# Optimization experiments

Measured on AMD Instinct MI355X. Metric: run time of the kernel, lower is better.

Reference implementation:

```python
import jax, jax.numpy as jnp
import numpy as np

N_EMBED = 1024
N_HEADS = 16
HEAD_DIM = N_EMBED // N_HEADS


def setup_inputs() -> dict:
    key = jax.random.key(0)
    ks = jax.random.split(key, 5)
    B, T, C = 4, 2048, N_EMBED
    s_in = 1.0 / np.sqrt(C)
    x = jax.random.normal(ks[0], (B, T, C), dtype=jnp.float32)
    W_qkv = jax.random.normal(ks[1], (C, 3 * C), dtype=jnp.float32) * s_in
    b_qkv = jnp.zeros((3 * C,), dtype=jnp.float32)
    W_out = jax.random.normal(ks[2], (C, C), dtype=jnp.float32) * s_in
    b_out = jnp.zeros((C,), dtype=jnp.float32)
    return {"x": x, "W_qkv": W_qkv, "b_qkv": b_qkv, "W_out": W_out, "b_out": b_out}


def reference(x, W_qkv, b_qkv, W_out, b_out):
    B, T, C = x.shape
    H, D = N_HEADS, HEAD_DIM
    qkv = x @ W_qkv + b_qkv                       # [B,T,3C]
    q, k, v = jnp.split(qkv, 3, axis=-1)
    # [B,T,C] -> [B,H,T,D]
    q = q.reshape(B, T, H, D).transpose(0, 2, 1, 3)
    k = k.reshape(B, T, H, D).transpose(0, 2, 1, 3)
    v = v.reshape(B, T, H, D).transpose(0, 2, 1, 3)
    scale = 1.0 / np.sqrt(D)
    attn = jnp.einsum('bhqd,bhkd->bhqk', q, k) * scale   # [B,H,T,T]
    causal = jnp.tril(jnp.ones((T, T), dtype=bool))
    attn = jnp.where(causal, attn, -jnp.inf)
    attn = jax.nn.softmax(attn, axis=-1)
    out = jnp.einsum('bhqk,bhkd->bhqd', attn, v)          # [B,H,T,D]
    out = out.transpose(0, 2, 1, 3).reshape(B, T, C)
    return out @ W_out + b_out
```

## Files before the change

kernel.cpp:

```cpp
#include <hip/hip_runtime.h>
#include <stdint.h>

#define BB 4
#define TT 2048
#define CC 1024
#define HH 16
#define DD 64
#define MM (BB*TT)

typedef __bf16 bf16x8 __attribute__((ext_vector_type(8)));
typedef float  f32x4  __attribute__((ext_vector_type(4)));

__device__ __forceinline__ unsigned short f2bf(float f) {
  __bf16 h = (__bf16)f;
  union { __bf16 h; unsigned short u; } c; c.h = h;
  return c.u;
}

__device__ __forceinline__ void glds16(const void* g, void* l) {
  __builtin_amdgcn_global_load_lds((const __attribute__((address_space(1))) void*)g,
                                   (__attribute__((address_space(3))) void*)l,
                                   16, 0, 0);
}

__device__ __forceinline__ int xcd_swz(int bid, int nwg) {
  if (nwg & 7) return bid;
  return (bid & 7) * (nwg >> 3) + (bid >> 3);
}

typedef unsigned short u16x8 __attribute__((ext_vector_type(8)));
__global__ void f32_to_bf16_kn(const float* __restrict__ in,
                               unsigned short* __restrict__ out, int n) {
  int i = (blockIdx.x * blockDim.x + threadIdx.x) * 8;
  const int stride = gridDim.x * blockDim.x * 8;
  for (; i < n; i += stride) {
    float4 a = *(const float4*)&in[i];
    float4 b = *(const float4*)&in[i + 4];
    u16x8 t;
    t[0]=f2bf(a.x); t[1]=f2bf(a.y); t[2]=f2bf(a.z); t[3]=f2bf(a.w);
    t[4]=f2bf(b.x); t[5]=f2bf(b.y); t[6]=f2bf(b.z); t[7]=f2bf(b.w);
    *(u16x8*)&out[i] = t;
  }
}

__global__ void transpose_to_bf16(const float* __restrict__ in,
                                  unsigned short* __restrict__ out,
                                  int R, int Cc) {
  __shared__ float tile[32][33];
  const int c0 = blockIdx.x * 32, r0 = blockIdx.y * 32;
  const int tx = threadIdx.x & 31, ty = threadIdx.x >> 5;
#pragma unroll
  for (int i = 0; i < 32; i += 8)
    tile[ty + i][tx] = in[(size_t)(r0 + ty + i) * Cc + c0 + tx];
  __syncthreads();
#pragma unroll
  for (int i = 0; i < 32; i += 8)
    out[(size_t)(c0 + ty + i) * R + r0 + tx] = f2bf(tile[tx][ty + i]);
}

template<int MODE>
__global__ void gemm128(const unsigned short* __restrict__ A,
                        const unsigned short* __restrict__ Bt,
                        const float* __restrict__ bias,
                        void* __restrict__ outp,
                        int M, int N, int K)
{
  __shared__ unsigned short Alds[128 * 32];
  __shared__ unsigned short Blds[128 * 32];
  const int tid = threadIdx.x;
  const int lane = tid & 63;
  const int wid  = tid >> 6;
  const int wm = wid >> 1, wn = wid & 1;
  const int nwg = (int)(gridDim.x * gridDim.y);
  const int swz = xcd_swz((int)(blockIdx.y * gridDim.x + blockIdx.x), nwg);
  const int m0 = (swz / (int)gridDim.x) * 128;
  const int n0 = (swz % (int)gridDim.x) * 128;
  const int l15 = lane & 15, l4 = lane >> 4;

  f32x4 acc[4][4];
#pragma unroll
  for (int i = 0; i < 4; i++)
#pragma unroll
    for (int j = 0; j < 4; j++) acc[i][j] = (f32x4){0.f, 0.f, 0.f, 0.f};

  for (int k0 = 0; k0 < K; k0 += 32) {
    __syncthreads();
#pragma unroll
    for (int c = 0; c < 2; ++c) {
      const int chunk = wid * 2 + c;
      const int linear = chunk * 1024 + lane * 16;
      const int row  = linear >> 6;
      const int colb = linear & 63;
      glds16((const char*)A  + ((size_t)(m0 + row) * K + k0) * 2 + colb,
             (char*)Alds + chunk * 1024);
      glds16((const char*)Bt + ((size_t)(n0 + row) * K + k0) * 2 + colb,
             (char*)Blds + chunk * 1024);
    }
    __syncthreads();
    bf16x8 af[4], bfr[4];
#pragma unroll
    for (int i = 0; i < 4; i++)
      af[i]  = *(const bf16x8*)&Alds[(wm * 64 + i * 16 + l15) * 32 + l4 * 8];
#pragma unroll
    for (int j = 0; j < 4; j++)
      bfr[j] = *(const bf16x8*)&Blds[(wn * 64 + j * 16 + l15) * 32 + l4 * 8];
#pragma unroll
    for (int i = 0; i < 4; i++)
#pragma unroll
      for (int j = 0; j < 4; j++)
        acc[i][j] = __builtin_amdgcn_mfma_f32_16x16x32_bf16(af[i], bfr[j], acc[i][j], 0, 0, 0);
  }

#pragma unroll
  for (int i = 0; i < 4; i++) {
#pragma unroll
    for (int j = 0; j < 4; j++) {
      const int n = n0 + wn * 64 + j * 16 + l15;
      const float bn = bias[n];
#pragma unroll
      for (int r = 0; r < 4; r++) {
        const int m = m0 + wm * 64 + i * 16 + l4 * 4 + r;
        float v = acc[i][j][r] + bn;
        if (MODE == 0) {
          unsigned short* qb = (unsigned short*)outp;
          const int which = n >> 10;
          const int cc = n & 1023;
          const int h = cc >> 6, d = cc & 63;
          const int b = m >> 11, t = m & 2047;
          if (which == 0) {
            const size_t off = (((size_t)(b * HH + h)) * TT + t) * DD + d;
            qb[off] = f2bf(v * 0.125f);
          } else if (which == 1) {
            const size_t off = (((size_t)(b * HH + h)) * TT + t) * DD + d;
            qb[(size_t)MM * CC + off] = f2bf(v);
          } else {
            const size_t offv = (((size_t)(b * HH + h)) * DD + d) * TT + t;
            qb[(size_t)2 * MM * CC + offv] = f2bf(v);
          }
        } else {
          float* O = (float*)outp;
          O[(size_t)m * N + n] = v;
        }
      }
    }
  }
}

__global__ void attn_fwd(const unsigned short* __restrict__ qbuf,
                         const unsigned short* __restrict__ kbuf,
                         const unsigned short* __restrict__ vtbuf,
                         unsigned short* __restrict__ ao)
{
  __shared__ unsigned short Klds[2][64 * 64];
  __shared__ unsigned short Vt[2][64 * 64];
  __shared__ unsigned short Plds[4 * 16 * 64];
  const int tid = threadIdx.x, lane = tid & 63, w = tid >> 6;
  const int l15 = lane & 15, l4 = lane >> 4;
  const int NQT = TT / 64;
  const int nwg = NQT * BB * HH;
  const int swz = xcd_swz((int)blockIdx.x, nwg);
  const int bh = swz / NQT;
  const int qtile = NQT - 1 - (swz % NQT);
  const int q0 = qtile * 64;
  const unsigned short* Qb  = qbuf  + (size_t)bh * TT * DD;
  const unsigned short* Kb  = kbuf  + (size_t)bh * TT * DD;
  const unsigned short* VTb = vtbuf + (size_t)bh * DD * TT;

  const int srow = lane >> 3;
  const int scol = ((lane & 7) ^ srow) * 8;

  bf16x8 qf[2];
#pragma unroll
  for (int ks = 0; ks < 2; ks++)
    qf[ks] = *(const bf16x8*)&Qb[(size_t)(q0 + w * 16 + l15) * DD + ks * 32 + l4 * 8];

  f32x4 o[4];
#pragma unroll
  for (int df = 0; df < 4; df++) o[df] = (f32x4){0.f, 0.f, 0.f, 0.f};
  float mrow[4] = {-__builtin_huge_valf(), -__builtin_huge_valf(),
                   -__builtin_huge_valf(), -__builtin_huge_valf()};
  float lrow[4] = {0.f, 0.f, 0.f, 0.f};

  const int qwmin = q0 + w * 16;
  const int nt = qtile + 1;

#pragma unroll
  for (int j = 0; j < 2; j++) {
    const int g = w * 2 + j;
    const int row = g * 8 + srow;
    glds16(Kb + (size_t)row * DD + scol,       (char*)&Klds[0][0] + g * 1024);
    glds16(VTb + (size_t)row * TT + scol,      (char*)&Vt[0][0]   + g * 1024);
  }

  for (int t = 0; t < nt; t++) {
    __syncthreads();
    if (t + 1 < nt) {
      const int kv1 = (t + 1) * 64;
      const int nb = (t + 1) & 1;
#pragma unroll
      for (int j = 0; j < 2; j++) {
        const int g = w * 2 + j;
        const int row = g * 8 + srow;
        glds16(Kb + (size_t)(kv1 + row) * DD + scol, (char*)&Klds[nb][0] + g * 1024);
        glds16(VTb + (size_t)row * TT + kv1 + scol,  (char*)&Vt[nb][0]   + g * 1024);
      }
    }
    const int cb = t & 1;
    const int kv0 = t * 64;

    f32x4 s[4];
#pragma unroll
    for (int fc = 0; fc < 4; fc++) {
      s[fc] = (f32x4){0.f, 0.f, 0.f, 0.f};
      const int kr = fc * 16 + l15;
#pragma unroll
      for (int ks = 0; ks < 2; ks++) {
        bf16x8 kf = *(const bf16x8*)&Klds[cb][(kr * 64 + ks * 32 + l4 * 8) ^ ((kr & 7) << 3)];
        s[fc] = __builtin_amdgcn_mfma_f32_16x16x32_bf16(qf[ks], kf, s[fc], 0, 0, 0);
      }
    }
    if (kv0 + 63 > qwmin) {
#pragma unroll
      for (int fc = 0; fc < 4; fc++)
#pragma unroll
        for (int r = 0; r < 4; r++) {
          const int kv = kv0 + fc * 16 + l15;
          const int q  = qwmin + l4 * 4 + r;
          if (kv > q) s[fc][r] = -__builtin_huge_valf();
        }
    }
    const int base = w * 1024;
#pragma unroll
    for (int r = 0; r < 4; r++) {
      float tm = fmaxf(fmaxf(s[0][r], s[1][r]), fmaxf(s[2][r], s[3][r]));
      tm = fmaxf(tm, __shfl_xor(tm, 1, 16));
      tm = fmaxf(tm, __shfl_xor(tm, 2, 16));
      tm = fmaxf(tm, __shfl_xor(tm, 4, 16));
      tm = fmaxf(tm, __shfl_xor(tm, 8, 16));
      const float mn = fmaxf(mrow[r], tm);
      const float sc = __expf(mrow[r] - mn);
      float p[4];
#pragma unroll
      for (int fc = 0; fc < 4; fc++) p[fc] = __expf(s[fc][r] - mn);
      float ps = (p[0] + p[1]) + (p[2] + p[3]);
      ps += __shfl_xor(ps, 1, 16);
      ps += __shfl_xor(ps, 2, 16);
      ps += __shfl_xor(ps, 4, 16);
      ps += __shfl_xor(ps, 8, 16);
      lrow[r] = lrow[r] * sc + ps;
      mrow[r] = mn;
#pragma unroll
      for (int df = 0; df < 4; df++) o[df][r] *= sc;
      const int ro = l4 * 4 + r;
#pragma unroll
      for (int fc = 0; fc < 4; fc++)
        Plds[base + ((ro * 64 + fc * 16 + l15) ^ ((ro & 7) << 3))] = f2bf(p[fc]);
    }
    bf16x8 pa[2];
#pragma unroll
    for (int ks = 0; ks < 2; ks++)
      pa[ks] = *(const bf16x8*)&Plds[base + ((l15 * 64 + ks * 32 + l4 * 8) ^ ((l15 & 7) << 3))];
#pragma unroll
    for (int df = 0; df < 4; df++) {
      const int d = df * 16 + l15;
#pragma unroll
      for (int ks = 0; ks < 2; ks++) {
        bf16x8 vf = *(const bf16x8*)&Vt[cb][(d * 64 + ks * 32 + l4 * 8) ^ ((d & 7) << 3)];
        o[df] = __builtin_amdgcn_mfma_f32_16x16x32_bf16(pa[ks], vf, o[df], 0, 0, 0);
      }
    }
  }

  const int b = bh >> 4, h = bh & 15;
#pragma unroll
  for (int r = 0; r < 4; r++) {
    const float inv = 1.0f / lrow[r];
    const int q = qwmin + l4 * 4 + r;
#pragma unroll
    for (int df = 0; df < 4; df++) {
      const int d = df * 16 + l15;
      ao[((size_t)(b * TT + q)) * CC + h * DD + d] = f2bf(o[df][r] * inv);
    }
  }
}

extern "C" void kernel_launch(void* const* d_in, const int* in_sizes, int n_in,
                              void* d_out, int out_size, void* d_ws, size_t ws_size,
                              hipStream_t stream) {
  const float* x    = (const float*)d_in[0];
  const float* Wqkv = (const float*)d_in[1];
  const float* bqkv = (const float*)d_in[2];
  const float* Wout = (const float*)d_in[3];
  const float* bout = (const float*)d_in[4];
  float* out = (float*)d_out;
  char* ws = (char*)d_ws;

  unsigned short* xb    = (unsigned short*)ws;
  unsigned short* wqkvt = (unsigned short*)(ws + 16777216);
  unsigned short* woutt = (unsigned short*)(ws + 23068672);
  unsigned short* qkv   = (unsigned short*)(ws + 25165824);
  unsigned short* ao    = xb;

  f32_to_bf16_kn<<<2048, 256, 0, stream>>>(x, xb, MM * CC);
  transpose_to_bf16<<<dim3(3 * CC / 32, CC / 32), 256, 0, stream>>>(Wqkv, wqkvt, CC, 3 * CC);
  transpose_to_bf16<<<dim3(CC / 32, CC / 32), 256, 0, stream>>>(Wout, woutt, CC, CC);

  gemm128<0><<<dim3(3 * CC / 128, MM / 128), 256, 0, stream>>>(
      xb, wqkvt, bqkv, (void*)qkv, MM, 3 * CC, CC);

  attn_fwd<<<(TT / 64) * BB * HH, 256, 0, stream>>>(
      qkv, qkv + (size_t)MM * CC, qkv + (size_t)2 * MM * CC, ao);

  gemm128<1><<<dim3(CC / 128, MM / 128), 256, 0, stream>>>(
      ao, woutt, bout, (void*)out, MM, CC, CC);
}
```

Before: 338.1 us.

## Transpose attention MFMAs and shuffle P via permlane swaps instead of LDS

Swaps the MFMA operand order so each lane holds one query row's scores. This reduces the softmax row reductions to two cross-lane shuffles, with a single running max and sum per lane. The P matrix is repacked into the PV operand layout with v_permlane32/16_swap instead of a round trip through shared memory, which removes the Plds buffer. The change also skips fully masked KV tiles per wave and raises wave priority around the MFMA blocks. The risk is correctness of the permlane layout mapping, and the output store is now strided in the column dimension.

After: 297.6 us. -12.0%, faster.

```diff
diff --git a/kernel.cpp b/kernel.cpp
--- a/kernel.cpp
+++ b/kernel.cpp
@@ -21,6 +21,13 @@
   __builtin_amdgcn_global_load_lds((const __attribute__((address_space(1))) void*)g,
                                    (__attribute__((address_space(3))) void*)l,
                                    16, 0, 0);
+}
+
+__device__ __forceinline__ void perm32swap(uint32_t& a, uint32_t& b) {
+  asm volatile("v_permlane32_swap_b32 %0, %1" : "+v"(a), "+v"(b));
+}
+__device__ __forceinline__ void perm16swap(uint32_t& a, uint32_t& b) {
+  asm volatile("v_permlane16_swap_b32 %0, %1" : "+v"(a), "+v"(b));
 }
 
 __device__ __forceinline__ int xcd_swz(int bid, int nwg) {
@@ -153,7 +160,6 @@
 {
   __shared__ unsigned short Klds[2][64 * 64];
   __shared__ unsigned short Vt[2][64 * 64];
-  __shared__ unsigned short Plds[4 * 16 * 64];
   const int tid = threadIdx.x, lane = tid & 63, w = tid >> 6;
   const int l15 = lane & 15, l4 = lane >> 4;
   const int NQT = TT / 64;
@@ -177,11 +183,11 @@
   f32x4 o[4];
 #pragma unroll
   for (int df = 0; df < 4; df++) o[df] = (f32x4){0.f, 0.f, 0.f, 0.f};
-  float mrow[4] = {-__builtin_huge_valf(), -__builtin_huge_valf(),
-                   -__builtin_huge_valf(), -__builtin_huge_valf()};
-  float lrow[4] = {0.f, 0.f, 0.f, 0.f};
+  float m_st = -__builtin_huge_valf();
+  float l_st = 0.f;
 
   const int qwmin = q0 + w * 16;
+  const int qrow  = qwmin + l15;
   const int nt = qtile + 1;
 
 #pragma unroll
@@ -208,80 +214,90 @@
     const int cb = t & 1;
     const int kv0 = t * 64;
 
-    f32x4 s[4];
-#pragma unroll
-    for (int fc = 0; fc < 4; fc++) {
-      s[fc] = (f32x4){0.f, 0.f, 0.f, 0.f};
-      const int kr = fc * 16 + l15;
+    if (kv0 <= qwmin + 15) {
+      f32x4 s[4];
+      __builtin_amdgcn_s_setprio(1);
+#pragma unroll
+      for (int fc = 0; fc < 4; fc++) {
+        s[fc] = (f32x4){0.f, 0.f, 0.f, 0.f};
+        const int kr = fc * 16 + l15;
+#pragma unroll
+        for (int ks = 0; ks < 2; ks++) {
+          bf16x8 kf = *(const bf16x8*)&Klds[cb][(kr * 64 + ks * 32 + l4 * 8) ^ ((kr & 7) << 3)];
+          s[fc] = __builtin_amdgcn_mfma_f32_16x16x32_bf16(kf, qf[ks], s[fc], 0, 0, 0);
+        }
+      }
+      __builtin_amdgcn_s_setprio(0);
+      if (kv0 + 63 > qwmin) {
+#pragma unroll
+        for (int fc = 0; fc < 4; fc++)
+#pragma unroll
+          for (int r = 0; r < 4; r++)
+            if (kv0 + fc * 16 + l4 * 4 + r > qrow) s[fc][r] = -__builtin_huge_valf();
+      }
+      float tm = s[0][0];
+#pragma unroll
+      for (int fc = 0; fc < 4; fc++)
+#pragma unroll
+        for (int r = 0; r < 4; r++) tm = fmaxf(tm, s[fc][r]);
+      tm = fmaxf(tm, __shfl_xor(tm, 16));
+      tm = fmaxf(tm, __shfl_xor(tm, 32));
+      const float mn = fmaxf(m_st, tm);
+      const float sc = __expf(m_st - mn);
+      m_st = mn;
+      float rs = 0.f;
+      uint32_t wpk[4][2];
+#pragma unroll
+      for (int fc = 0; fc < 4; fc++) {
+        float p0 = __expf(s[fc][0] - mn), p1 = __expf(s[fc][1] - mn);
+        float p2 = __expf(s[fc][2] - mn), p3 = __expf(s[fc][3] - mn);
+        rs += (p0 + p1) + (p2 + p3);
+        union { unsigned short u[2]; uint32_t d; } a, b;
+        a.u[0] = f2bf(p0); a.u[1] = f2bf(p1);
+        b.u[0] = f2bf(p2); b.u[1] = f2bf(p3);
+        wpk[fc][0] = a.d; wpk[fc][1] = b.d;
+      }
+      rs += __shfl_xor(rs, 16);
+      rs += __shfl_xor(rs, 32);
+      l_st = l_st * sc + rs;
+#pragma unroll
+      for (int df = 0; df < 4; df++)
+#pragma unroll
+        for (int r = 0; r < 4; r++) o[df][r] *= sc;
+      bf16x8 pa[2];
 #pragma unroll
       for (int ks = 0; ks < 2; ks++) {
-        bf16x8 kf = *(const bf16x8*)&Klds[cb][(kr * 64 + ks * 32 + l4 * 8) ^ ((kr & 7) << 3)];
-        s[fc] = __builtin_amdgcn_mfma_f32_16x16x32_bf16(qf[ks], kf, s[fc], 0, 0, 0);
-      }
-    }
-    if (kv0 + 63 > qwmin) {
-#pragma unroll
-      for (int fc = 0; fc < 4; fc++)
-#pragma unroll
-        for (int r = 0; r < 4; r++) {
-          const int kv = kv0 + fc * 16 + l15;
-          const int q  = qwmin + l4 * 4 + r;
-          if (kv > q) s[fc][r] = -__builtin_huge_valf();
+        uint32_t Aq = wpk[2 * ks][0], Bq = wpk[2 * ks][1];
+        uint32_t Cq = wpk[2 * ks + 1][0], Dq = wpk[2 * ks + 1][1];
+        perm32swap(Aq, Cq); perm16swap(Aq, Cq);
+        perm32swap(Bq, Dq); perm16swap(Bq, Dq);
+        union { uint32_t d[4]; bf16x8 v; } pf;
+        pf.d[0] = Aq; pf.d[1] = Bq; pf.d[2] = Cq; pf.d[3] = Dq;
+        pa[ks] = pf.v;
+      }
+      __builtin_amdgcn_s_setprio(1);
+#pragma unroll
+      for (int df = 0; df < 4; df++) {
+        const int d = df * 16 + l15;
+#pragma unroll
+        for (int ks = 0; ks < 2; ks++) {
+          bf16x8 vf = *(const bf16x8*)&Vt[cb][(d * 64 + ks * 32 + l4 * 8) ^ ((d & 7) << 3)];
+          o[df] = __builtin_amdgcn_mfma_f32_16x16x32_bf16(vf, pa[ks], o[df], 0, 0, 0);
         }
-    }
-    const int base = w * 1024;
+      }
+      __builtin_amdgcn_s_setprio(0);
+    }
+  }
+
+  const int b = bh >> 4, h = bh & 15;
+  const float inv = 1.0f / l_st;
+#pragma unroll
+  for (int df = 0; df < 4; df++)
 #pragma unroll
     for (int r = 0; r < 4; r++) {
-      float tm = fmaxf(fmaxf(s[0][r], s[1][r]), fmaxf(s[2][r], s[3][r]));
-      tm = fmaxf(tm, __shfl_xor(tm, 1, 16));
-      tm = fmaxf(tm, __shfl_xor(tm, 2, 16));
-      tm = fmaxf(tm, __shfl_xor(tm, 4, 16));
-      tm = fmaxf(tm, __shfl_xor(tm, 8, 16));
-      const float mn = fmaxf(mrow[r], tm);
-      const float sc = __expf(mrow[r] - mn);
-      float p[4];
-#pragma unroll
-      for (int fc = 0; fc < 4; fc++) p[fc] = __expf(s[fc][r] - mn);
-      float ps = (p[0] + p[1]) + (p[2] + p[3]);
-      ps += __shfl_xor(ps, 1, 16);
-      ps += __shfl_xor(ps, 2, 16);
-      ps += __shfl_xor(ps, 4, 16);
-      ps += __shfl_xor(ps, 8, 16);
-      lrow[r] = lrow[r] * sc + ps;
-      mrow[r] = mn;
-#pragma unroll
-      for (int df = 0; df < 4; df++) o[df][r] *= sc;
-      const int ro = l4 * 4 + r;
-#pragma unroll
-      for (int fc = 0; fc < 4; fc++)
-        Plds[base + ((ro * 64 + fc * 16 + l15) ^ ((ro & 7) << 3))] = f2bf(p[fc]);
-    }
-    bf16x8 pa[2];
-#pragma unroll
-    for (int ks = 0; ks < 2; ks++)
-      pa[ks] = *(const bf16x8*)&Plds[base + ((l15 * 64 + ks * 32 + l4 * 8) ^ ((l15 & 7) << 3))];
-#pragma unroll
-    for (int df = 0; df < 4; df++) {
-      const int d = df * 16 + l15;
-#pragma unroll
-      for (int ks = 0; ks < 2; ks++) {
-        bf16x8 vf = *(const bf16x8*)&Vt[cb][(d * 64 + ks * 32 + l4 * 8) ^ ((d & 7) << 3)];
-        o[df] = __builtin_amdgcn_mfma_f32_16x16x32_bf16(pa[ks], vf, o[df], 0, 0, 0);
-      }
-    }
-  }
-
-  const int b = bh >> 4, h = bh & 15;
-#pragma unroll
-  for (int r = 0; r < 4; r++) {
-    const float inv = 1.0f / lrow[r];
-    const int q = qwmin + l4 * 4 + r;
-#pragma unroll
-    for (int df = 0; df < 4; df++) {
-      const int d = df * 16 + l15;
-      ao[((size_t)(b * TT + q)) * CC + h * DD + d] = f2bf(o[df][r] * inv);
-    }
-  }
+      const int d = df * 16 + l4 * 4 + r;
+      ao[((size_t)(b * TT + qrow)) * CC + h * DD + d] = f2bf(o[df][r] * inv);
+    }
 }
 
 extern "C" void kernel_launch(void* const* d_in, const int* in_sizes, int n_in,
```
